# Optimization experiments

Hardware: AMD Instinct MI355X
Metric: run time of the kernel (lower is better)

Reference implementation:

```python
import jax, jax.numpy as jnp
import numpy as np

N = 65536
D_MODEL = 8
D_STATE = 16
D_INNER = 16  # d_model * expand
PK = 12       # sqrt(144)
NE = 144
EH = 16
GH = 4
NH = 4
PEER_IN = GH + 2 * D_MODEL + 2   # 22
GRU_IN = 2 + 2 * D_MODEL          # 18
RESCALE = 0.1


def setup_inputs() -> dict:
    key = jax.random.key(0)
    ks = iter(jax.random.split(key, 40))
    rn = lambda shape, s=0.02: jax.random.normal(next(ks), shape, dtype=jnp.float32) * s
    inp = {
        'grad': jax.random.normal(next(ks), (N,), dtype=jnp.float32),
        'sharpness': jax.random.uniform(next(ks), (N,), dtype=jnp.float32),
        'gru_state': jnp.zeros((N, GH), jnp.float32),
        'mfwd_state': jnp.zeros((D_INNER, D_STATE), jnp.float32),
        'mbwd_state': jnp.zeros((D_INNER, D_STATE), jnp.float32),
        # input_proj: Linear(2, d_model, bias=True)
        'inproj_W': rn((D_MODEL, 2), 0.5), 'inproj_b': jnp.zeros((D_MODEL,), jnp.float32),
        # two Mamba3ScanBlocks stacked on leading axis: [0]=fwd, [1]=bwd
        'm_inW': rn((2, 2 * D_INNER, D_MODEL), 0.2),
        'm_dtW': rn((2, D_INNER, D_INNER), 0.2), 'm_dtb': jnp.zeros((2, D_INNER), jnp.float32),
        'm_BW': rn((2, D_STATE, D_INNER), 0.2), 'm_CW': rn((2, D_STATE, D_INNER), 0.2),
        'm_Alog': jnp.broadcast_to(jnp.log(jnp.linspace(1.0, D_STATE, D_STATE, dtype=jnp.float32))[None, None, :], (2, D_INNER, D_STATE)).copy(),
        'm_D': jnp.ones((2, D_INNER), jnp.float32),
        'm_rope': rn((2, D_INNER, D_STATE), 0.01),
        'm_outW': rn((2, D_MODEL, D_INNER), 0.2),
        # MiniGRU: Linear(22, 4) x3
        'gru_Wz': rn((GH, GRU_IN + GH), 0.2), 'gru_bz': jnp.zeros((GH,), jnp.float32),
        'gru_Wr': rn((GH, GRU_IN + GH), 0.2), 'gru_br': jnp.zeros((GH,), jnp.float32),
        'gru_Wh': rn((GH, GRU_IN + GH), 0.2), 'gru_bh': jnp.zeros((GH,), jnp.float32),
        # PEER heads (stacked over heads)
        'peer_qW': rn((NH, D_MODEL, PEER_IN), 0.2),
        'keysA': rn((NH, PK, D_MODEL // 2), 0.02),
        'keysB': rn((NH, PK, D_MODEL // 2), 0.02),
        # shared expert pool
        'eW1': rn((NE, EH, 1), 0.02), 'eb1': jnp.zeros((NE, EH), jnp.float32),
        'eW2': rn((NE, 1, EH), 0.02), 'eb2': jnp.zeros((NE, 1), jnp.float32),
    }
    return inp


def _mamba_scan(x, h0, inW, dtW, dtb, BW, CW, Alog, Dp, rope, outW):
    # x: [N, d_model]; h0: [d_inner, d_state]
    xz = x @ inW.T                       # [N, 2*d_inner]
    xb, z = xz[:, :D_INNER], xz[:, D_INNER:]
    dt = jax.nn.softplus(xb @ dtW.T + dtb)   # [N, d_inner]
    B = xb @ BW.T                            # [N, d_state]
    C = xb @ CW.T                            # [N, d_state]
    A = -jnp.exp(Alog)                       # [d_inner, d_state]

    def step(h, t):
        dt_i, B_i, C_i, xb_i = t
        dti = dt_i[:, None]                                # [d_inner, 1]
        A_bar = (1.0 + dti * A * 0.5) / (1.0 - dti * A * 0.5 + 1e-8)
        ph = dti * rope
        h_rot = h * jnp.cos(ph) - jnp.roll(h, 1, axis=-1) * jnp.sin(ph)
        h_new = A_bar * h_rot + (dti * B_i[None, :]) * xb_i[:, None]
        y = (h_new * C_i[None, :]).sum(-1)                 # [d_inner]
        return h_new, y

    h_final, ys = jax.lax.scan(step, h0, (dt, B, C, xb))
    y = ys * jax.nn.silu(z) + Dp[None, :] * xb
    return y @ outW.T, h_final


def reference(grad, sharpness, gru_state, mfwd_state, mbwd_state,
              inproj_W, inproj_b,
              m_inW, m_dtW, m_dtb, m_BW, m_CW, m_Alog, m_D, m_rope, m_outW,
              gru_Wz, gru_bz, gru_Wr, gru_br, gru_Wh, gru_bh,
              peer_qW, keysA, keysB, eW1, eb1, eW2, eb2):
    g = grad.reshape(-1).astype(jnp.float32)
    s = sharpness.reshape(-1).astype(jnp.float32)
    sort_idx = jnp.argsort(jnp.abs(g))
    gs, ss = g[sort_idx], s[sort_idx]

    x = jnp.stack([gs, ss], axis=-1) @ inproj_W.T + inproj_b   # [N, d_model]

    fwd_out, new_fwd = _mamba_scan(x, mfwd_state, m_inW[0], m_dtW[0], m_dtb[0],
                                   m_BW[0], m_CW[0], m_Alog[0], m_D[0], m_rope[0], m_outW[0])
    bwd_out, new_bwd = _mamba_scan(x[::-1], mbwd_state, m_inW[1], m_dtW[1], m_dtb[1],
                                   m_BW[1], m_CW[1], m_Alog[1], m_D[1], m_rope[1], m_outW[1])
    bwd_out = bwd_out[::-1]

    unsort = jnp.argsort(sort_idx)
    fwd_ctx = fwd_out[unsort]
    bwd_ctx = bwd_out[unsort]

    # MiniGRU
    gru_in = jnp.concatenate([g[:, None], s[:, None], fwd_ctx, bwd_ctx], axis=-1)  # [N, 18]
    h = gru_state.astype(jnp.float32)
    xh = jnp.concatenate([gru_in, h], axis=-1)
    zg = jax.nn.sigmoid(xh @ gru_Wz.T + gru_bz)
    r = jax.nn.sigmoid(xh @ gru_Wr.T + gru_br)
    xrh = jnp.concatenate([gru_in, r * h], axis=-1)
    h_t = jnp.tanh(xrh @ gru_Wh.T + gru_bh)
    new_gru = (1.0 - zg) * h + zg * h_t

    # PEER routing (4 heads, product keys)
    peer_in = jnp.concatenate([new_gru, fwd_ctx, bwd_ctx, g[:, None], s[:, None]], axis=-1)  # [N, 22]
    half = D_MODEL // 2
    total = jnp.zeros((g.shape[0], 1), jnp.float32)
    for hidx in range(NH):
        q = peer_in @ peer_qW[hidx].T                              # [N, d_model]
        idx_a = jnp.argmax(q[:, :half] @ keysA[hidx].T, axis=-1)   # [N]
        idx_b = jnp.argmax(q[:, half:] @ keysB[hidx].T, axis=-1)
        eidx = idx_a * PK + idx_b                                  # [N]
        z1 = jax.nn.relu(eW1[eidx][:, :, 0] * g[:, None] + eb1[eidx])   # [N, EH]
        out = (eW2[eidx][:, 0, :] * z1).sum(-1, keepdims=True) + eb2[eidx]
        total = total + out
    total = total / NH

    smart_grad = g + RESCALE * total[:, 0]
    return smart_grad.reshape(grad.shape), new_gru, new_fwd, new_bwd
```

## Files before the change

kernel.cpp:

```cpp
#include <hip/hip_runtime.h>
#include <math.h>

#define NTOT 65536
#define LCH 128
#define WRM 32
#define TILE 32
#define CCH 512
#define NBK 256
#define CAP2 512

__device__ __forceinline__ float d_softplus(float x){
  return fmaxf(x, 0.f) + __logf(1.f + __expf(-fabsf(x)));
}
__device__ __forceinline__ float d_sigmoid(float x){
  return 1.f / (1.f + __expf(-x));
}
__device__ __forceinline__ float fast_rcp(float x){
  return __builtin_amdgcn_rcpf(x);
}
template<int CTRL>
__device__ __forceinline__ float dpp_mov(float x){
  return __int_as_float(__builtin_amdgcn_update_dpp(0, __float_as_int(x), CTRL, 0xF, 0xF, true));
}

__device__ __forceinline__ float erfinv_f(float x){
  float w = -__logf((1.0f - x) * (1.0f + x));
  float p;
  if (w < 5.0f){
    w = w - 2.5f;
    p = 2.81022636e-08f;
    p = fmaf(p, w, 3.43273939e-07f);
    p = fmaf(p, w, -3.5233877e-06f);
    p = fmaf(p, w, -4.39150654e-06f);
    p = fmaf(p, w, 0.00021858087f);
    p = fmaf(p, w, -0.00125372503f);
    p = fmaf(p, w, -0.00417768164f);
    p = fmaf(p, w, 0.246640727f);
    p = fmaf(p, w, 1.50140941f);
  } else {
    w = sqrtf(w) - 3.0f;
    p = -0.000200214257f;
    p = fmaf(p, w, 0.000100950558f);
    p = fmaf(p, w, 0.00134934322f);
    p = fmaf(p, w, -0.00367342844f);
    p = fmaf(p, w, 0.00573950773f);
    p = fmaf(p, w, -0.0076224613f);
    p = fmaf(p, w, 0.00943887047f);
    p = fmaf(p, w, 1.00167406f);
    p = fmaf(p, w, 2.83297682f);
  }
  return p * x;
}

__global__ __launch_bounds__(512) void k_bucketsort(
    const float* __restrict__ g, unsigned* __restrict__ sidx)
{
  __shared__ unsigned long long buf[CAP2];
  __shared__ unsigned sred[512];
  __shared__ unsigned scnt;
  int t = threadIdx.x, blk = blockIdx.x;
  int lane = t & 63;
  unsigned kLo, kHi;
  if (blk == 0) kLo = 0u;
  else          kLo = __float_as_uint(1.41421356f * erfinv_f((float)blk * (1.0f/256.0f)));
  if (blk == NBK-1) kHi = 0x80000000u;
  else              kHi = __float_as_uint(1.41421356f * erfinv_f((float)(blk+1) * (1.0f/256.0f)));
  if (t == 0) scnt = 0u;
  __syncthreads();
  unsigned below_loc = 0;
  const float4* g4 = (const float4*)g;
  for (int r = 0; r < 32; ++r){
    int rr = (r + (blk & 31)) & 31;
    int i4 = rr*512 + t;
    float4 v = g4[i4];
    unsigned kk[4];
    kk[0] = __float_as_uint(v.x) & 0x7fffffffu;
    kk[1] = __float_as_uint(v.y) & 0x7fffffffu;
    kk[2] = __float_as_uint(v.z) & 0x7fffffffu;
    kk[3] = __float_as_uint(v.w) & 0x7fffffffu;
    unsigned idx0 = (unsigned)i4 * 4u;
    #pragma unroll
    for (int q = 0; q < 4; ++q){
      unsigned key = kk[q];
      below_loc += (key < kLo) ? 1u : 0u;
      bool in = (key >= kLo) && (key < kHi);
      unsigned long long mask = __ballot(in);
      if (in){
        unsigned prefix = (unsigned)__popcll(mask & ((1ull << lane) - 1ull));
        unsigned basep = 0u;
        if (prefix == 0u) basep = atomicAdd(&scnt, (unsigned)__popcll(mask));
        int leader = __ffsll((long long)mask) - 1;
        basep = __shfl(basep, leader, 64);
        unsigned p = basep + prefix;
        if (p < CAP2) buf[p] = ((unsigned long long)key << 16) | (idx0 + (unsigned)q);
      }
    }
  }
  sred[t] = below_loc;
  __syncthreads();
  unsigned cnt = scnt;
  if (cnt > CAP2) cnt = CAP2;
  for (int off = 256; off > 0; off >>= 1){
    if (t < off) sred[t] += sred[t + off];
    __syncthreads();
  }
  unsigned base = sred[0];
  if ((unsigned)t < cnt){
    unsigned long long val = buf[t];
    unsigned pos = 0u;
    for (unsigned m = 0; m < cnt; ++m)
      pos += (buf[m] < val) ? 1u : 0u;
    sidx[base + pos] = (unsigned)(val & 0xFFFFull);
  }
}

__global__ __launch_bounds__(512, 4) void k_mega(
    const float* __restrict__ g, const float* __restrict__ sh,
    const unsigned* __restrict__ sidx,
    const float* __restrict__ inprojW, const float* __restrict__ inprojb,
    const float* __restrict__ m_inW, const float* __restrict__ m_dtW,
    const float* __restrict__ m_dtb, const float* __restrict__ m_BW,
    const float* __restrict__ m_CW,
    const float* __restrict__ Alog, const float* __restrict__ rope,
    const float* __restrict__ m_D, const float* __restrict__ m_outW,
    const float* __restrict__ mfwd, const float* __restrict__ mbwd,
    const float* __restrict__ gru_state,
    const float* __restrict__ Wz, const float* __restrict__ bz,
    const float* __restrict__ Wr, const float* __restrict__ br,
    const float* __restrict__ Wh, const float* __restrict__ bh,
    const float* __restrict__ qW, const float* __restrict__ kA, const float* __restrict__ kB,
    const float* __restrict__ eW1, const float* __restrict__ eb1,
    const float* __restrict__ eW2, const float* __restrict__ eb2,
    float* __restrict__ dout)
{
  __shared__ float wip[16], wipb[8];
  __shared__ float win2[576], wdt2[544], wB2[544], wC2[544], wdtb2[32], wOW2[256];
  __shared__ float gsAll[(LCH + 2*WRM)*2];
  __shared__ float4 PKL[2*TILE*17];
  __shared__ float2 SBL[2*TILE*17];
  __shared__ float xbL[2*TILE*17];
  __shared__ float ldsV[2*TILE*17];
  __shared__ float ctxT[2*LCH*9];
  __shared__ float sWz[88], sWr[88], sWh[88], sbz[4], sbr[4], sbh[4];
  __shared__ float sqW[704], skA[192], skB[192];
  __shared__ float hsum[LCH*4];

  int c = blockIdx.x;
  int t = threadIdx.x;
  int dir = t >> 8;
  int tt = t & 255;
  int d = tt >> 4, s = tt & 15;
  int p8 = tt >> 3, w8 = tt & 7;

  if (t < 16) wip[t] = inprojW[t];
  if (t < 8)  wipb[t] = inprojb[t];
  { int dd = t >> 8, k = t & 255;
    win2[dd*288 + (k>>3)*9 + (k&7)]   = m_inW[t];
    wdt2[dd*272 + (k>>4)*17 + (k&15)] = m_dtW[t];
    wB2 [dd*272 + (k>>4)*17 + (k&15)] = m_BW[t];
    wC2 [dd*272 + (k>>4)*17 + (k&15)] = m_CW[t];
  }
  if (t < 32)  wdtb2[t] = m_dtb[t];
  if (t < 256) wOW2[t]  = m_outW[t];
  for (int k = t; k < 88; k += 512){ sWz[k]=Wz[k]; sWr[k]=Wr[k]; sWh[k]=Wh[k]; }
  if (t < 4){ sbz[t]=bz[t]; sbr[t]=br[t]; sbh[t]=bh[t]; }
  for (int k = t; k < 704; k += 512) sqW[k]=qW[k];
  for (int k = t; k < 192; k += 512){ skA[k]=kA[k]; skB[k]=kB[k]; }

  int base = c*LCH - WRM;
  for (int k = t; k < LCH + 2*WRM; k += 512){
    int p = base + k;
    p = p < 0 ? 0 : (p >= NTOT ? NTOT-1 : p);
    unsigned u = sidx[p];
    gsAll[k*2]   = g[u];
    gsAll[k*2+1] = sh[u];
  }

  float Ah = -__expf(Alog[dir*256 + tt]) * 0.5f;
  float rp = rope[dir*256 + tt];
  float Dd = m_D[dir*16 + d];
  bool fwd = (dir == 0);
  bool bnd = (fwd && c == 0) || (!fwd && c == CCH-1);
  float h = 0.f;
  const float* winp = &win2[dir*288];
  const float* wdtp = &wdt2[dir*272];
  const float* wBp  = &wB2[dir*272];
  const float* wCp  = &wC2[dir*272];
  __syncthreads();

  const int T = (LCH + WRM) / TILE;
  const int warmT = WRM / TILE;
  for (int j = 0; j < T; ++j){
    int lo = fwd ? (base + j*TILE) : (base + (LCH + 2*WRM) - (j+1)*TILE);
    int loff = lo - base;
    float zreg[2];
    {
      float gg = gsAll[(loff + p8)*2], ss = gsAll[(loff + p8)*2 + 1];
      float x[8];
      #pragma unroll
      for (int m = 0; m < 8; ++m)
        x[m] = fmaf(wip[m*2], gg, fmaf(wip[m*2+1], ss, wipb[m]));
      #pragma unroll
      for (int kk = 0; kk < 2; ++kk){
        int k = w8*2 + kk;
        float a = 0.f, zz = 0.f;
        #pragma unroll
        for (int m = 0; m < 8; ++m){
          a  += winp[k*9+m]*x[m];
          zz += winp[(16+k)*9+m]*x[m];
        }
        xbL[(dir*TILE + p8)*17 + k] = a;
        zreg[kk] = zz;
      }
    }
    __syncthreads();
    {
      float xb16[16];
      #pragma unroll
      for (int m = 0; m < 16; ++m) xb16[m] = xbL[(dir*TILE + p8)*17 + m];
      #pragma unroll
      for (int kk = 0; kk < 2; ++kk){
        int k = w8*2 + kk;
        float u = wdtb2[dir*16+k], ba = 0.f, ca = 0.f;
        #pragma unroll
        for (int m = 0; m < 16; ++m){
          float xm = xb16[m];
          u  += wdtp[k*17+m]*xm;
          ba += wBp[k*17+m]*xm;
          ca += wCp[k*17+m]*xm;
        }
        float dt = d_softplus(u);
        float zz = zreg[kk];
        float sz = zz * d_sigmoid(zz);
        PKL[(dir*TILE + p8)*17 + k] = make_float4(dt, dt*xb16[k], sz, xb16[k]);
        SBL[(dir*TILE + p8)*17 + k] = make_float2(ba, ca);
      }
    }
    __syncthreads();
    if (j == warmT && bnd) h = fwd ? mfwd[tt] : mbwd[tt];
    bool real = (j >= warmT);
    for (int mb = (j == 0 ? TILE/8 : 0); mb < TILE/4; ++mb){
      float yv[4];
      #pragma unroll
      for (int q = 0; q < 4; ++q){
        int m = mb*4 + q;
        int lm = fwd ? m : TILE-1 - m;
        float4 dd = PKL[(dir*TILE + lm)*17 + d];
        float2 sv = SBL[(dir*TILE + lm)*17 + s];
        float dt = dd.x, dxb = dd.y;
        float xh = dt * Ah;
        float Ab = (1.f + xh) * fast_rcp(1.f - xh + 1e-8f);
        float ph = dt * rp;
        float p2 = ph * ph;
        float ccos = 1.f - p2*(0.5f - 0.041666668f*p2);
        float ssin = ph*(1.f - 0.16666667f*p2);
        float a = Ab * ccos;
        float b = -Ab * ssin;
        float hm = dpp_mov<0x121>(h);
        h = fmaf(a, h, fmaf(b, hm, dxb * sv.x));
        if (real){
          float v = h * sv.y;
          v += dpp_mov<0xB1>(v);
          v += dpp_mov<0x4E>(v);
          v += dpp_mov<0x140>(v);
          v += dpp_mov<0x141>(v);
          yv[q] = fmaf(v, dd.z, Dd * dd.w);
        }
      }
      if (real && s < 4){
        float val = (s == 0) ? yv[0] : ((s == 1) ? yv[1] : ((s == 2) ? yv[2] : yv[3]));
        int p = fwd ? (mb*4 + s) : (TILE-1 - (mb*4 + s));
        ldsV[(dir*TILE + p)*17 + d] = val;
      }
    }
    __syncthreads();
    if (real){
      int pos = tt >> 3, m = tt & 7;
      float a = 0.f;
      #pragma unroll
      for (int k = 0; k < 16; ++k) a += wOW2[dir*128 + m*16 + k]*ldsV[(dir*TILE + pos)*17 + k];
      ctxT[(dir*LCH + (lo - c*LCH + pos))*9 + m] = a;
    }
  }
  if (fwd && c == CCH-1)  dout[5*NTOT + tt] = h;
  if (!fwd && c == 0)     dout[5*NTOT + 256 + tt] = h;
  __syncthreads();

  {
    int elem = t >> 2, sub = t & 3;
    unsigned u = sidx[c*LCH + elem];
    float gi = gsAll[(WRM + elem)*2], si = gsAll[(WRM + elem)*2 + 1];
    float xin[22];
    xin[0] = gi; xin[1] = si;
    #pragma unroll
    for (int m = 0; m < 8; ++m){
      xin[2+m]  = ctxT[elem*9 + m];
      xin[10+m] = ctxT[(LCH + elem)*9 + m];
    }
    float hg[4];
    #pragma unroll
    for (int k = 0; k < 4; ++k) hg[k] = gru_state[u*4 + k];
    float zg[4], rg[4];
    #pragma unroll
    for (int o = 0; o < 4; ++o){
      float az = sbz[o], ar2 = sbr[o];
      #pragma unroll
      for (int cc = 0; cc < 18; ++cc){ az += sWz[o*22+cc]*xin[cc]; ar2 += sWr[o*22+cc]*xin[cc]; }
      #pragma unroll
      for (int cc = 0; cc < 4; ++cc){ az += sWz[o*22+18+cc]*hg[cc]; ar2 += sWr[o*22+18+cc]*hg[cc]; }
      zg[o] = d_sigmoid(az);
      rg[o] = d_sigmoid(ar2);
    }
    float ng[4];
    #pragma unroll
    for (int o = 0; o < 4; ++o){
      float ah = sbh[o];
      #pragma unroll
      for (int cc = 0; cc < 18; ++cc) ah += sWh[o*22+cc]*xin[cc];
      #pragma unroll
      for (int cc = 0; cc < 4; ++cc) ah += sWh[o*22+18+cc]*(rg[cc]*hg[cc]);
      float ht = tanhf(ah);
      ng[o] = (1.f - zg[o])*hg[o] + zg[o]*ht;
    }
    if (sub == 0){
      #pragma unroll
      for (int k = 0; k < 4; ++k) dout[NTOT + u*4 + k] = ng[k];
    }
    float pin[22];
    #pragma unroll
    for (int k = 0; k < 4; ++k) pin[k] = ng[k];
    #pragma unroll
    for (int m = 0; m < 16; ++m) pin[4+m] = xin[2+m];
    pin[20] = gi; pin[21] = si;
    int hh = sub;
    float qv[8];
    #pragma unroll
    for (int o = 0; o < 8; ++o){
      float a = 0.f;
      #pragma unroll
      for (int cc = 0; cc < 22; ++cc) a += sqW[hh*176 + o*22 + cc]*pin[cc];
      qv[o] = a;
    }
    int ia = 0; float best = -1e30f;
    #pragma unroll
    for (int k = 0; k < 12; ++k){
      float sc = 0.f;
      #pragma unroll
      for (int m = 0; m < 4; ++m) sc += skA[hh*48 + k*4 + m]*qv[m];
      if (sc > best){ best = sc; ia = k; }
    }
    int ib = 0; best = -1e30f;
    #pragma unroll
    for (int k = 0; k < 12; ++k){
      float sc = 0.f;
      #pragma unroll
      for (int m = 0; m < 4; ++m) sc += skB[hh*48 + k*4 + m]*qv[4+m];
      if (sc > best){ best = sc; ib = k; }
    }
    int e = ia*12 + ib;
    float outv = eb2[e];
    #pragma unroll
    for (int u16 = 0; u16 < 16; ++u16){
      float z1 = fmaxf(eW1[e*16+u16]*gi + eb1[e*16+u16], 0.f);
      outv += eW2[e*16+u16]*z1;
    }
    hsum[elem*4 + sub] = outv;
  }
  __syncthreads();
  if (t < LCH){
    float total = (hsum[t*4] + hsum[t*4+1] + hsum[t*4+2] + hsum[t*4+3])*0.25f;
    unsigned u = sidx[c*LCH + t];
    float gi = gsAll[(WRM + t)*2];
    dout[u] = gi + 0.1f*total;
  }
}

extern "C" void kernel_launch(void* const* d_in, const int* in_sizes, int n_in,
                              void* d_out, int out_size, void* d_ws, size_t ws_size,
                              hipStream_t stream)
{
  const float* grad     = (const float*)d_in[0];
  const float* sharp    = (const float*)d_in[1];
  const float* gru_st   = (const float*)d_in[2];
  const float* mfwd     = (const float*)d_in[3];
  const float* mbwd     = (const float*)d_in[4];
  const float* inprojW  = (const float*)d_in[5];
  const float* inprojb  = (const float*)d_in[6];
  const float* m_inW    = (const float*)d_in[7];
  const float* m_dtW    = (const float*)d_in[8];
  const float* m_dtb    = (const float*)d_in[9];
  const float* m_BW     = (const float*)d_in[10];
  const float* m_CW     = (const float*)d_in[11];
  const float* m_Alog   = (const float*)d_in[12];
  const float* m_D      = (const float*)d_in[13];
  const float* m_rope   = (const float*)d_in[14];
  const float* m_outW   = (const float*)d_in[15];
  const float* gWz      = (const float*)d_in[16];
  const float* gbz      = (const float*)d_in[17];
  const float* gWr      = (const float*)d_in[18];
  const float* gbr      = (const float*)d_in[19];
  const float* gWh      = (const float*)d_in[20];
  const float* gbh      = (const float*)d_in[21];
  const float* peer_qW  = (const float*)d_in[22];
  const float* keysA    = (const float*)d_in[23];
  const float* keysB    = (const float*)d_in[24];
  const float* eW1      = (const float*)d_in[25];
  const float* eb1      = (const float*)d_in[26];
  const float* eW2      = (const float*)d_in[27];
  const float* eb2      = (const float*)d_in[28];
  float* out = (float*)d_out;

  unsigned* sidx = (unsigned*)d_ws;

  k_bucketsort<<<NBK, 512, 0, stream>>>(grad, sidx);
  k_mega<<<CCH, 512, 0, stream>>>(grad, sharp, sidx,
      inprojW, inprojb, m_inW, m_dtW, m_dtb, m_BW, m_CW,
      m_Alog, m_rope, m_D, m_outW, mfwd, mbwd, gru_st,
      gWz, gbz, gWr, gbr, gWh, gbh, peer_qW, keysA, keysB,
      eW1, eb1, eW2, eb2, out);
}
```

Measured before the change: 202.5 us.

## Fold Mamba projections into composite weights and template-unroll scan tiles

Precomputes composite weight matrices (dt/B/C times in_proj), so each position's projections become 8-wide dots from the input embedding. This removes the intermediate xb staging buffer and one barrier per tile. The scan loop becomes a fully unrolled template per direction and warm/real phase, with the D skip term folded into the packed data. The GRU is restructured so each of the 4 sub-threads computes one gate output and exchanges values via DPP, and it uses a cheaper tanh. Expert and weight loads are vectorised to float4, at the cost of extra per-block setup work and small floating-point reassociation differences.

```diff
diff --git a/kernel.cpp b/kernel.cpp
--- a/kernel.cpp
+++ b/kernel.cpp
@@ -18,9 +18,23 @@
 __device__ __forceinline__ float fast_rcp(float x){
   return __builtin_amdgcn_rcpf(x);
 }
+__device__ __forceinline__ float cheap_tanh(float x){
+  float e = __expf(2.f*x);
+  return fmaf(-2.f, fast_rcp(e + 1.f), 1.f);
+}
 template<int CTRL>
 __device__ __forceinline__ float dpp_mov(float x){
   return __int_as_float(__builtin_amdgcn_update_dpp(0, __float_as_int(x), CTRL, 0xF, 0xF, true));
+}
+
+__device__ __forceinline__ float dot8(const float* w, const float x[8], float acc){
+  const float4* w4 = (const float4*)w;
+  float4 a = w4[0], b = w4[1];
+  acc = fmaf(a.x, x[0], acc); acc = fmaf(a.y, x[1], acc);
+  acc = fmaf(a.z, x[2], acc); acc = fmaf(a.w, x[3], acc);
+  acc = fmaf(b.x, x[4], acc); acc = fmaf(b.y, x[5], acc);
+  acc = fmaf(b.z, x[6], acc); acc = fmaf(b.w, x[7], acc);
+  return acc;
 }
 
 __device__ __forceinline__ float erfinv_f(float x){
@@ -114,6 +128,40 @@
   }
 }
 
+template<bool FWD, bool REAL, int M0>
+__device__ __forceinline__ void scan_tile(float& h, const float4* __restrict__ pk,
+    const float2* __restrict__ sb, float* __restrict__ lv, float Ah, float rp, int s)
+{
+  float yv[4];
+  #pragma unroll
+  for (int m = M0; m < TILE; ++m){
+    const int lm = FWD ? m : (TILE-1 - m);
+    float4 dd = pk[lm*17];
+    float2 sv = sb[lm*17];
+    float dt = dd.x;
+    float xh = dt * Ah;
+    float Ab = (1.f + xh) * fast_rcp(1.f - xh + 1e-8f);
+    float ph = dt * rp, p2 = ph*ph;
+    float ccos = fmaf(-p2, fmaf(-0.041666668f, p2, 0.5f), 1.f);
+    float nsin = ph * fmaf(0.16666667f, p2, -1.f);
+    float hm = dpp_mov<0x121>(h);
+    h = fmaf(Ab*ccos, h, fmaf(Ab*nsin, hm, dd.y * sv.x));
+    if (REAL){
+      float v = h * sv.y;
+      v += dpp_mov<0xB1>(v);
+      v += dpp_mov<0x4E>(v);
+      v += dpp_mov<0x140>(v);
+      v += dpp_mov<0x141>(v);
+      yv[m & 3] = fmaf(v, dd.z, dd.w);
+      if ((m & 3) == 3 && s < 4){
+        float val = (s==0) ? yv[0] : ((s==1) ? yv[1] : ((s==2) ? yv[2] : yv[3]));
+        int p = FWD ? (m-3+s) : (TILE-1 - (m-3+s));
+        lv[p*20] = val;
+      }
+    }
+  }
+}
+
 __global__ __launch_bounds__(512, 4) void k_mega(
     const float* __restrict__ g, const float* __restrict__ sh,
     const unsigned* __restrict__ sidx,
@@ -134,13 +182,13 @@
     float* __restrict__ dout)
 {
   __shared__ float wip[16], wipb[8];
-  __shared__ float win2[576], wdt2[544], wB2[544], wC2[544], wdtb2[32], wOW2[256];
+  __shared__ float cXB[2*16*12], cDT[2*16*12], cB[2*16*12], cC[2*16*12], cZ[2*16*12];
+  __shared__ float wdtb2[32], sD2[32], wOW2[256];
   __shared__ float gsAll[(LCH + 2*WRM)*2];
   __shared__ float4 PKL[2*TILE*17];
   __shared__ float2 SBL[2*TILE*17];
-  __shared__ float xbL[2*TILE*17];
-  __shared__ float ldsV[2*TILE*17];
-  __shared__ float ctxT[2*LCH*9];
+  __shared__ float ldsV[2*TILE*20];
+  __shared__ float ctxT[2*LCH*12];
   __shared__ float sWz[88], sWr[88], sWh[88], sbz[4], sbr[4], sbh[4];
   __shared__ float sqW[704], skA[192], skB[192];
   __shared__ float hsum[LCH*4];
@@ -154,14 +202,24 @@
 
   if (t < 16) wip[t] = inprojW[t];
   if (t < 8)  wipb[t] = inprojb[t];
-  { int dd = t >> 8, k = t & 255;
-    win2[dd*288 + (k>>3)*9 + (k&7)]   = m_inW[t];
-    wdt2[dd*272 + (k>>4)*17 + (k&15)] = m_dtW[t];
-    wB2 [dd*272 + (k>>4)*17 + (k&15)] = m_BW[t];
-    wC2 [dd*272 + (k>>4)*17 + (k&15)] = m_CW[t];
-  }
-  if (t < 32)  wdtb2[t] = m_dtb[t];
-  if (t < 256) wOW2[t]  = m_outW[t];
+  if (t < 32){ wdtb2[t] = m_dtb[t]; sD2[t] = m_D[t]; }
+  if (t < 256) wOW2[t] = m_outW[t];
+  if (t < 256){
+    int dd2 = t >> 7, rem = t & 127, k = rem >> 3, m = rem & 7;
+    cXB[dd2*192 + k*12 + m] = m_inW[dd2*256 + k*8 + m];
+    cZ [dd2*192 + k*12 + m] = m_inW[dd2*256 + (16+k)*8 + m];
+  }
+  for (int idx = t; idx < 768; idx += 512){
+    int mat = idx >> 8, rem = idx & 255;
+    int dd2 = rem >> 7, k = (rem >> 3) & 15, m = rem & 7;
+    const float* wm = (mat==0) ? m_dtW : ((mat==1) ? m_BW : m_CW);
+    float a = 0.f;
+    #pragma unroll
+    for (int j2 = 0; j2 < 16; ++j2)
+      a = fmaf(wm[dd2*256 + k*16 + j2], m_inW[dd2*256 + j2*8 + m], a);
+    float* dst = (mat==0) ? cDT : ((mat==1) ? cB : cC);
+    dst[dd2*192 + k*12 + m] = a;
+  }
   for (int k = t; k < 88; k += 512){ sWz[k]=Wz[k]; sWr[k]=Wr[k]; sWh[k]=Wh[k]; }
   if (t < 4){ sbz[t]=bz[t]; sbr[t]=br[t]; sbh[t]=bh[t]; }
   for (int k = t; k < 704; k += 512) sqW[k]=qW[k];
@@ -178,108 +236,64 @@
 
   float Ah = -__expf(Alog[dir*256 + tt]) * 0.5f;
   float rp = rope[dir*256 + tt];
-  float Dd = m_D[dir*16 + d];
   bool fwd = (dir == 0);
   bool bnd = (fwd && c == 0) || (!fwd && c == CCH-1);
   float h = 0.f;
-  const float* winp = &win2[dir*288];
-  const float* wdtp = &wdt2[dir*272];
-  const float* wBp  = &wB2[dir*272];
-  const float* wCp  = &wC2[dir*272];
+  const float4* pkB = &PKL[dir*TILE*17 + d];
+  const float2* sbB = &SBL[dir*TILE*17 + s];
+  float* lvB = &ldsV[dir*TILE*20 + d];
   __syncthreads();
 
-  const int T = (LCH + WRM) / TILE;
-  const int warmT = WRM / TILE;
-  for (int j = 0; j < T; ++j){
+  auto do_proj = [&](int loff){
+    float gg = gsAll[(loff + p8)*2], ss = gsAll[(loff + p8)*2 + 1];
+    float x[8];
+    #pragma unroll
+    for (int m = 0; m < 8; ++m)
+      x[m] = fmaf(wip[m*2], gg, fmaf(wip[m*2+1], ss, wipb[m]));
+    #pragma unroll
+    for (int kk = 0; kk < 2; ++kk){
+      int k = w8*2 + kk;
+      int wb = dir*192 + k*12;
+      float xb  = dot8(&cXB[wb], x, 0.f);
+      float dtp = dot8(&cDT[wb], x, wdtb2[dir*16 + k]);
+      float zz  = dot8(&cZ [wb], x, 0.f);
+      float bb  = dot8(&cB [wb], x, 0.f);
+      float ccv = dot8(&cC [wb], x, 0.f);
+      float dtv = d_softplus(dtp);
+      float sz  = zz * d_sigmoid(zz);
+      PKL[(dir*TILE + p8)*17 + k] = make_float4(dtv, dtv*xb, sz, sD2[dir*16 + k]*xb);
+      SBL[(dir*TILE + p8)*17 + k] = make_float2(bb, ccv);
+    }
+  };
+
+  {
+    int loff = fwd ? 0 : (LCH + 2*WRM) - TILE;
+    do_proj(loff);
+    __syncthreads();
+    if (fwd) scan_tile<true,  false, TILE/2>(h, pkB, sbB, lvB, Ah, rp, s);
+    else     scan_tile<false, false, TILE/2>(h, pkB, sbB, lvB, Ah, rp, s);
+    __syncthreads();
+    if (bnd) h = fwd ? mfwd[tt] : mbwd[tt];
+  }
+  for (int j = 1; j < 5; ++j){
     int lo = fwd ? (base + j*TILE) : (base + (LCH + 2*WRM) - (j+1)*TILE);
-    int loff = lo - base;
-    float zreg[2];
-    {
-      float gg = gsAll[(loff + p8)*2], ss = gsAll[(loff + p8)*2 + 1];
-      float x[8];
-      #pragma unroll
-      for (int m = 0; m < 8; ++m)
-        x[m] = fmaf(wip[m*2], gg, fmaf(wip[m*2+1], ss, wipb[m]));
-      #pragma unroll
-      for (int kk = 0; kk < 2; ++kk){
-        int k = w8*2 + kk;
-        float a = 0.f, zz = 0.f;
-        #pragma unroll
-        for (int m = 0; m < 8; ++m){
-          a  += winp[k*9+m]*x[m];
-          zz += winp[(16+k)*9+m]*x[m];
-        }
-        xbL[(dir*TILE + p8)*17 + k] = a;
-        zreg[kk] = zz;
-      }
-    }
+    do_proj(lo - base);
+    __syncthreads();
+    if (fwd) scan_tile<true,  true, 0>(h, pkB, sbB, lvB, Ah, rp, s);
+    else     scan_tile<false, true, 0>(h, pkB, sbB, lvB, Ah, rp, s);
     __syncthreads();
     {
-      float xb16[16];
-      #pragma unroll
-      for (int m = 0; m < 16; ++m) xb16[m] = xbL[(dir*TILE + p8)*17 + m];
-      #pragma unroll
-      for (int kk = 0; kk < 2; ++kk){
-        int k = w8*2 + kk;
-        float u = wdtb2[dir*16+k], ba = 0.f, ca = 0.f;
-        #pragma unroll
-        for (int m = 0; m < 16; ++m){
-          float xm = xb16[m];
-          u  += wdtp[k*17+m]*xm;
-          ba += wBp[k*17+m]*xm;
-          ca += wCp[k*17+m]*xm;
-        }
-        float dt = d_softplus(u);
-        float zz = zreg[kk];
-        float sz = zz * d_sigmoid(zz);
-        PKL[(dir*TILE + p8)*17 + k] = make_float4(dt, dt*xb16[k], sz, xb16[k]);
-        SBL[(dir*TILE + p8)*17 + k] = make_float2(ba, ca);
-      }
-    }
-    __syncthreads();
-    if (j == warmT && bnd) h = fwd ? mfwd[tt] : mbwd[tt];
-    bool real = (j >= warmT);
-    for (int mb = (j == 0 ? TILE/8 : 0); mb < TILE/4; ++mb){
-      float yv[4];
-      #pragma unroll
-      for (int q = 0; q < 4; ++q){
-        int m = mb*4 + q;
-        int lm = fwd ? m : TILE-1 - m;
-        float4 dd = PKL[(dir*TILE + lm)*17 + d];
-        float2 sv = SBL[(dir*TILE + lm)*17 + s];
-        float dt = dd.x, dxb = dd.y;
-        float xh = dt * Ah;
-        float Ab = (1.f + xh) * fast_rcp(1.f - xh + 1e-8f);
-        float ph = dt * rp;
-        float p2 = ph * ph;
-        float ccos = 1.f - p2*(0.5f - 0.041666668f*p2);
-        float ssin = ph*(1.f - 0.16666667f*p2);
-        float a = Ab * ccos;
-        float b = -Ab * ssin;
-        float hm = dpp_mov<0x121>(h);
-        h = fmaf(a, h, fmaf(b, hm, dxb * sv.x));
-        if (real){
-          float v = h * sv.y;
-          v += dpp_mov<0xB1>(v);
-          v += dpp_mov<0x4E>(v);
-          v += dpp_mov<0x140>(v);
-          v += dpp_mov<0x141>(v);
-          yv[q] = fmaf(v, dd.z, Dd * dd.w);
-        }
-      }
-      if (real && s < 4){
-        float val = (s == 0) ? yv[0] : ((s == 1) ? yv[1] : ((s == 2) ? yv[2] : yv[3]));
-        int p = fwd ? (mb*4 + s) : (TILE-1 - (mb*4 + s));
-        ldsV[(dir*TILE + p)*17 + d] = val;
-      }
-    }
-    __syncthreads();
-    if (real){
-      int pos = tt >> 3, m = tt & 7;
+      int pos = tt >> 3, mm = tt & 7;
+      const float4* lr = (const float4*)&ldsV[(dir*TILE + pos)*20];
+      const float4* wr = (const float4*)&wOW2[dir*128 + mm*16];
       float a = 0.f;
       #pragma unroll
-      for (int k = 0; k < 16; ++k) a += wOW2[dir*128 + m*16 + k]*ldsV[(dir*TILE + pos)*17 + k];
-      ctxT[(dir*LCH + (lo - c*LCH + pos))*9 + m] = a;
+      for (int k4 = 0; k4 < 4; ++k4){
+        float4 lv4 = lr[k4]; float4 w4 = wr[k4];
+        a = fmaf(w4.x, lv4.x, a); a = fmaf(w4.y, lv4.y, a);
+        a = fmaf(w4.z, lv4.z, a); a = fmaf(w4.w, lv4.w, a);
+      }
+      ctxT[(dir*LCH + (lo - c*LCH + pos))*12 + mm] = a;
     }
   }
   if (fwd && c == CCH-1)  dout[5*NTOT + tt] = h;
@@ -290,79 +304,77 @@
     int elem = t >> 2, sub = t & 3;
     unsigned u = sidx[c*LCH + elem];
     float gi = gsAll[(WRM + elem)*2], si = gsAll[(WRM + elem)*2 + 1];
-    float xin[22];
+    float xin[18];
     xin[0] = gi; xin[1] = si;
     #pragma unroll
     for (int m = 0; m < 8; ++m){
-      xin[2+m]  = ctxT[elem*9 + m];
-      xin[10+m] = ctxT[(LCH + elem)*9 + m];
-    }
-    float hg[4];
-    #pragma unroll
-    for (int k = 0; k < 4; ++k) hg[k] = gru_state[u*4 + k];
-    float zg[4], rg[4];
-    #pragma unroll
-    for (int o = 0; o < 4; ++o){
-      float az = sbz[o], ar2 = sbr[o];
+      xin[2+m]  = ctxT[elem*12 + m];
+      xin[10+m] = ctxT[(LCH + elem)*12 + m];
+    }
+    float4 hv = *(const float4*)&gru_state[u*4u];
+    int wb = sub*22;
+    float az = sbz[sub], ar = sbr[sub], ah = sbh[sub];
+    #pragma unroll
+    for (int cc = 0; cc < 18; ++cc){
+      az = fmaf(sWz[wb+cc], xin[cc], az);
+      ar = fmaf(sWr[wb+cc], xin[cc], ar);
+      ah = fmaf(sWh[wb+cc], xin[cc], ah);
+    }
+    az += sWz[wb+18]*hv.x + sWz[wb+19]*hv.y + sWz[wb+20]*hv.z + sWz[wb+21]*hv.w;
+    ar += sWr[wb+18]*hv.x + sWr[wb+19]*hv.y + sWr[wb+20]*hv.z + sWr[wb+21]*hv.w;
+    float zg = d_sigmoid(az), rg = d_sigmoid(ar);
+    float h01 = (sub & 1) ? hv.y : hv.x;
+    float h23 = (sub & 1) ? hv.w : hv.z;
+    float hown = (sub & 2) ? h23 : h01;
+    float rh  = rg * hown;
+    float rh1 = dpp_mov<0xB1>(rh);
+    float rh2 = dpp_mov<0x4E>(rh);
+    float rh3 = dpp_mov<0x4E>(rh1);
+    int s1 = sub^1, s2 = sub^2, s3 = sub^3;
+    ah += sWh[wb+18+sub]*rh + sWh[wb+18+s1]*rh1 + sWh[wb+18+s2]*rh2 + sWh[wb+18+s3]*rh3;
+    float ht  = cheap_tanh(ah);
+    float ngo = fmaf(zg, ht - hown, hown);
+    dout[NTOT + u*4u + (unsigned)sub] = ngo;
+    float n1 = dpp_mov<0xB1>(ngo);
+    float n2 = dpp_mov<0x4E>(ngo);
+    float n3 = dpp_mov<0x4E>(n1);
+    float qv[8];
+    #pragma unroll
+    for (int o = 0; o < 8; ++o){
+      int qb = sub*176 + o*22;
+      float a = sqW[qb+sub]*ngo + sqW[qb+s1]*n1 + sqW[qb+s2]*n2 + sqW[qb+s3]*n3;
       #pragma unroll
-      for (int cc = 0; cc < 18; ++cc){ az += sWz[o*22+cc]*xin[cc]; ar2 += sWr[o*22+cc]*xin[cc]; }
-      #pragma unroll
-      for (int cc = 0; cc < 4; ++cc){ az += sWz[o*22+18+cc]*hg[cc]; ar2 += sWr[o*22+18+cc]*hg[cc]; }
-      zg[o] = d_sigmoid(az);
-      rg[o] = d_sigmoid(ar2);
-    }
-    float ng[4];
-    #pragma unroll
-    for (int o = 0; o < 4; ++o){
-      float ah = sbh[o];
-      #pragma unroll
-      for (int cc = 0; cc < 18; ++cc) ah += sWh[o*22+cc]*xin[cc];
-      #pragma unroll
-      for (int cc = 0; cc < 4; ++cc) ah += sWh[o*22+18+cc]*(rg[cc]*hg[cc]);
-      float ht = tanhf(ah);
-      ng[o] = (1.f - zg[o])*hg[o] + zg[o]*ht;
-    }
-    if (sub == 0){
-      #pragma unroll
-      for (int k = 0; k < 4; ++k) dout[NTOT + u*4 + k] = ng[k];
-    }
-    float pin[22];
-    #pragma unroll
-    for (int k = 0; k < 4; ++k) pin[k] = ng[k];
-    #pragma unroll
-    for (int m = 0; m < 16; ++m) pin[4+m] = xin[2+m];
-    pin[20] = gi; pin[21] = si;
-    int hh = sub;
-    float qv[8];
-    #pragma unroll
-    for (int o = 0; o < 8; ++o){
-      float a = 0.f;
-      #pragma unroll
-      for (int cc = 0; cc < 22; ++cc) a += sqW[hh*176 + o*22 + cc]*pin[cc];
+      for (int m2 = 0; m2 < 16; ++m2) a = fmaf(sqW[qb+4+m2], xin[2+m2], a);
+      a = fmaf(sqW[qb+20], gi, fmaf(sqW[qb+21], si, a));
       qv[o] = a;
     }
     int ia = 0; float best = -1e30f;
     #pragma unroll
     for (int k = 0; k < 12; ++k){
-      float sc = 0.f;
-      #pragma unroll
-      for (int m = 0; m < 4; ++m) sc += skA[hh*48 + k*4 + m]*qv[m];
+      int kb = sub*48 + k*4;
+      float sc = skA[kb]*qv[0] + skA[kb+1]*qv[1] + skA[kb+2]*qv[2] + skA[kb+3]*qv[3];
       if (sc > best){ best = sc; ia = k; }
     }
     int ib = 0; best = -1e30f;
     #pragma unroll
     for (int k = 0; k < 12; ++k){
-      float sc = 0.f;
-      #pragma unroll
-      for (int m = 0; m < 4; ++m) sc += skB[hh*48 + k*4 + m]*qv[4+m];
+      int kb = sub*48 + k*4;
+      float sc = skB[kb]*qv[4] + skB[kb+1]*qv[5] + skB[kb+2]*qv[6] + skB[kb+3]*qv[7];
       if (sc > best){ best = sc; ib = k; }
     }
     int e = ia*12 + ib;
     float outv = eb2[e];
-    #pragma unroll
-    for (int u16 = 0; u16 < 16; ++u16){
-      float z1 = fmaxf(eW1[e*16+u16]*gi + eb1[e*16+u16], 0.f);
-      outv += eW2[e*16+u16]*z1;
+    const float4* w14 = (const float4*)&eW1[e*16];
+    const float4* b14 = (const float4*)&eb1[e*16];
+    const float4* w24 = (const float4*)&eW2[e*16];
+    #pragma unroll
+    for (int q4 = 0; q4 < 4; ++q4){
+      float4 a1 = w14[q4], a2 = b14[q4], a3 = w24[q4];
+      float z1;
+      z1 = fmaxf(fmaf(a1.x, gi, a2.x), 0.f); outv = fmaf(a3.x, z1, outv);
+      z1 = fmaxf(fmaf(a1.y, gi, a2.y), 0.f); outv = fmaf(a3.y, z1, outv);
+      z1 = fmaxf(fmaf(a1.z, gi, a2.z), 0.f); outv = fmaf(a3.z, z1, outv);
+      z1 = fmaxf(fmaf(a1.w, gi, a2.w), 0.f); outv = fmaf(a3.w, z1, outv);
     }
     hsum[elem*4 + sub] = outv;
   }
```

Result: faster. 178.8 us (-11.7%).
